# Kernel tuning notes

Hardware: AMD Instinct MI355X
Metric: run time of the kernel (lower is better)

## Reference

```python
import jax, jax.numpy as jnp
import numpy as np

IN, OUT, R, ALPHA = 4096, 4096, 32, 32
SCALE = ALPHA / R

def setup_inputs() -> dict:
    key = jax.random.key(0)
    k1, k2, k3, k4, k5 = jax.random.split(key, 5)
    x = jax.random.normal(k1, (4, 2048, IN), dtype=jnp.float32)
    weight = jax.random.normal(k2, (OUT, IN), dtype=jnp.float32) * 0.02
    bias = jax.random.normal(k3, (OUT,), dtype=jnp.float32) * 0.02
    A = jax.random.normal(k4, (OUT, R), dtype=jnp.float32) * 0.01
    # original init is zeros; use small randn so the LoRA path is nontrivial
    B = jax.random.normal(k5, (IN, R), dtype=jnp.float32) * 0.01
    return {"x": x, "weight": weight, "bias": bias, "A": A, "B": B}

def reference(x, weight, bias, A, B):
    # delta_w = A @ B.T * (alpha/r); y = x @ (W + delta_w).T + bias
    delta_w = (A @ B.T) * SCALE            # [out, in]
    w_eff = weight + delta_w
    return jnp.einsum('bsi,oi->bso', x, w_eff) + bias
```

## Files before the change

kernel.cpp:

```cpp
#include <hip/hip_runtime.h>

#define IN_DIM 4096
#define OUT_DIM 4096
#define M_DIM 8192
#define RANK 32
#define BK 64
#define NT (IN_DIM / BK)

typedef __bf16 bf16x8 __attribute__((ext_vector_type(8)));
typedef float f32x4 __attribute__((ext_vector_type(4)));

__device__ __forceinline__ unsigned short f2bf(float f) {
  unsigned u = __builtin_bit_cast(unsigned, f);
  u += 0x7FFF + ((u >> 16) & 1);
  return (unsigned short)(u >> 16);
}

__global__ __launch_bounds__(256) void prep_kernel(
    const float* __restrict__ X, unsigned short* __restrict__ Xb,
    const float* __restrict__ W, const float* __restrict__ A,
    const float* __restrict__ B, unsigned short* __restrict__ Wb) {
  const int tid = threadIdx.x;
  if (blockIdx.x >= 1024) {
    const int idx0 = (blockIdx.x - 1024) * 256 + tid;
    const int stride = 512 * 256;
    const int total4 = (M_DIM * IN_DIM) / 4;
    for (int i = idx0; i < total4; i += stride) {
      const float4 v = reinterpret_cast<const float4*>(X)[i];
      ushort4 o;
      o.x = f2bf(v.x); o.y = f2bf(v.y); o.z = f2bf(v.z); o.w = f2bf(v.w);
      reinterpret_cast<ushort4*>(Xb)[i] = o;
    }
    return;
  }
  __shared__ unsigned short sA[128][40];
  __shared__ unsigned short sB[128][40];
  const int lane = tid & 63;
  const int wid  = tid >> 6;
  const int wr   = wid >> 1, wc = wid & 1;
  const int li   = lane & 15, kg = lane >> 4;
  const int bRow = (blockIdx.x >> 5) * 128;
  const int bCol = (blockIdx.x & 31) * 128;

  for (int i = tid; i < 128 * 8; i += 256) {
    const int r = i >> 3, q = i & 7;
    const float4 va = reinterpret_cast<const float4*>(A + (size_t)(bRow + r) * RANK)[q];
    ushort4 oa;
    oa.x = f2bf(va.x); oa.y = f2bf(va.y); oa.z = f2bf(va.z); oa.w = f2bf(va.w);
    *reinterpret_cast<ushort4*>(&sA[r][q * 4]) = oa;
    const float4 vb = reinterpret_cast<const float4*>(B + (size_t)(bCol + r) * RANK)[q];
    ushort4 ob;
    ob.x = f2bf(vb.x); ob.y = f2bf(vb.y); ob.z = f2bf(vb.z); ob.w = f2bf(vb.w);
    *reinterpret_cast<ushort4*>(&sB[r][q * 4]) = ob;
  }
  __syncthreads();

  bf16x8 af[4], bq[4];
#pragma unroll
  for (int m = 0; m < 4; ++m)
    af[m] = *reinterpret_cast<const bf16x8*>(&sA[wr * 64 + m * 16 + li][kg * 8]);
#pragma unroll
  for (int n = 0; n < 4; ++n)
    bq[n] = *reinterpret_cast<const bf16x8*>(&sB[wc * 64 + n * 16 + li][kg * 8]);

  f32x4 acc[4][4];
#pragma unroll
  for (int m = 0; m < 4; ++m)
#pragma unroll
    for (int n = 0; n < 4; ++n) {
      acc[m][n] = f32x4{0.f, 0.f, 0.f, 0.f};
      acc[m][n] = __builtin_amdgcn_mfma_f32_16x16x32_bf16(af[m], bq[n], acc[m][n], 0, 0, 0);
    }

#pragma unroll
  for (int m = 0; m < 4; ++m) {
#pragma unroll
    for (int n = 0; n < 4; ++n) {
      const int col = bCol + wc * 64 + n * 16 + li;
#pragma unroll
      for (int j = 0; j < 4; ++j) {
        const int row = bRow + wr * 64 + m * 16 + kg * 4 + j;
        const size_t idx = (size_t)row * IN_DIM + col;
        Wb[idx] = f2bf(W[idx] + acc[m][n][j]);
      }
    }
  }
}

__global__ __launch_bounds__(512, 2) void gemm_kernel(
    const unsigned short* __restrict__ Xb, const unsigned short* __restrict__ Wb,
    const float* __restrict__ bias, float* __restrict__ Y) {
  __shared__ unsigned short lds[8][8192];
  const int tid  = threadIdx.x;
  const int lane = tid & 63;
  const int wid  = tid >> 6;
  const int wr   = wid >> 2;
  const int wc   = wid & 3;
  const int li   = lane & 15, kg = lane >> 4;

  const int bid = blockIdx.x;
  const int swz = (bid & 7) * 64 + (bid >> 3);
  const int bx  = swz & 15;
  const int by  = swz >> 4;
  const int bRow = by * 256, bCol = bx * 256;

  const int kcS = (tid & 7) ^ ((tid >> 3) & 7);
  const unsigned short* srcA[2][2];
  const unsigned short* srcB[2][2];
#pragma unroll
  for (int h = 0; h < 2; ++h)
#pragma unroll
    for (int l = 0; l < 2; ++l) {
      const int gA = l * 128 + h * 64 + (tid >> 3);
      const int gB = (l * 2 + (tid >> 8)) * 64 + h * 32 + ((tid >> 3) & 31);
      srcA[h][l] = Xb + (size_t)(bRow + gA) * IN_DIM + kcS * 8;
      srcB[h][l] = Wb + (size_t)(bCol + gB) * IN_DIM + kcS * 8;
    }
  char* const ldsRaw = (char*)&lds[0][0];

#define GLD(src, dstoff)                                                       \
  __builtin_amdgcn_global_load_lds(                                            \
      (const __attribute__((address_space(1))) unsigned int*)(src),            \
      (__attribute__((address_space(3))) unsigned int*)(ldsRaw + (dstoff)),    \
      16, 0, 0)
#define STAGE_A(s, h)                                                          \
  do {                                                                         \
    const int q_ = (((s) & 1) << 2) + (h);                                     \
    GLD(srcA[h][0] + (s) * BK, q_ * 16384 + tid * 16);                         \
    GLD(srcA[h][1] + (s) * BK, q_ * 16384 + 8192 + tid * 16);                  \
  } while (0)
#define STAGE_B(s, h)                                                          \
  do {                                                                         \
    const int q_ = (((s) & 1) << 2) + 2 + (h);                                 \
    GLD(srcB[h][0] + (s) * BK, q_ * 16384 + tid * 16);                         \
    GLD(srcB[h][1] + (s) * BK, q_ * 16384 + 8192 + tid * 16);                  \
  } while (0)
#define BAR() __builtin_amdgcn_s_barrier()

  const int rowAoff = (wr * 64 + li) * 64;
  const int rowBoff = (wc * 32 + li) * 64;
  int kx[2];
  kx[0] = ((0 * 4 + kg) ^ (li & 7)) * 8;
  kx[1] = ((1 * 4 + kg) ^ (li & 7)) * 8;

  bf16x8 af[4][2], bq[4][2];
  f32x4 acc[8][4];
#pragma unroll
  for (int m = 0; m < 8; ++m)
#pragma unroll
    for (int n = 0; n < 4; ++n) acc[m][n] = f32x4{0.f, 0.f, 0.f, 0.f};

#define RD_A(ms_)                                                              \
  do {                                                                         \
    const unsigned short* b_ = &lds[(dcur << 2) + (ms_)][0] + rowAoff;         \
    _Pragma("unroll") for (int mq = 0; mq < 4; ++mq)                           \
      _Pragma("unroll") for (int ks = 0; ks < 2; ++ks)                         \
        af[mq][ks] =                                                           \
            *reinterpret_cast<const bf16x8*>(b_ + mq * 1024 + kx[ks]);         \
  } while (0)
#define RD_B(ns_)                                                              \
  do {                                                                         \
    const unsigned short* b_ = &lds[(dcur << 2) + 2 + (ns_)][0] + rowBoff;     \
    _Pragma("unroll") for (int nq = 0; nq < 2; ++nq)                           \
      _Pragma("unroll") for (int ks = 0; ks < 2; ++ks)                         \
        bq[(ns_) * 2 + nq][ks] =                                               \
            *reinterpret_cast<const bf16x8*>(b_ + nq * 1024 + kx[ks]);         \
  } while (0)
#define MM(ms_, ns_)                                                           \
  do {                                                                         \
    __builtin_amdgcn_s_setprio(1);                                             \
    _Pragma("unroll") for (int mq = 0; mq < 4; ++mq)                           \
      _Pragma("unroll") for (int nq = 0; nq < 2; ++nq)                         \
        _Pragma("unroll") for (int ks = 0; ks < 2; ++ks)                       \
          acc[(ms_) * 4 + mq][(ns_) * 2 + nq] =                                \
              __builtin_amdgcn_mfma_f32_16x16x32_bf16(                         \
                  af[mq][ks], bq[(ns_) * 2 + nq][ks],                          \
                  acc[(ms_) * 4 + mq][(ns_) * 2 + nq], 0, 0, 0);               \
    __builtin_amdgcn_s_setprio(0);                                             \
  } while (0)

  STAGE_A(0, 0); STAGE_B(0, 0); STAGE_A(0, 1); STAGE_B(0, 1);
  STAGE_A(1, 0); STAGE_B(1, 0);
  asm volatile("s_waitcnt vmcnt(4)" ::: "memory");
  BAR();

  for (int t = 0; t < NT; ++t) {
    const int dcur = t & 1;
    const bool st1 = (t + 1 < NT), st2 = (t + 2 < NT);
    if (st1) { STAGE_B(t + 1, 1); STAGE_A(t + 1, 1); }
    RD_A(0); RD_B(0);
    BAR();
    MM(0, 0);
    RD_B(1);
    BAR();
    MM(0, 1);
    if (st2) STAGE_A(t + 2, 0);
    RD_A(1);
    BAR();
    MM(1, 0);
    if (st2) {
      STAGE_B(t + 2, 0);
      asm volatile("s_waitcnt vmcnt(4)" ::: "memory");
    } else {
      asm volatile("s_waitcnt vmcnt(0)" ::: "memory");
    }
    BAR();
    MM(1, 1);
  }
#undef GLD
#undef STAGE_A
#undef STAGE_B
#undef RD_A
#undef RD_B
#undef MM
#undef BAR

#pragma unroll
  for (int nf = 0; nf < 4; ++nf) {
    const int col = bCol + wc * 64 + nf * 16 + li;
    const float bv = bias[col];
#pragma unroll
    for (int mf = 0; mf < 8; ++mf) {
      const int row0 = bRow + wr * 128 + mf * 16 + kg * 4;
#pragma unroll
      for (int j = 0; j < 4; ++j)
        Y[(size_t)(row0 + j) * OUT_DIM + col] = acc[mf][nf][j] + bv;
    }
  }
}

extern "C" void kernel_launch(void* const* d_in, const int* in_sizes, int n_in,
                              void* d_out, int out_size, void* d_ws, size_t ws_size,
                              hipStream_t stream) {
  const float* x    = (const float*)d_in[0];
  const float* w    = (const float*)d_in[1];
  const float* bias = (const float*)d_in[2];
  const float* A    = (const float*)d_in[3];
  const float* B    = (const float*)d_in[4];
  float* y = (float*)d_out;

  const size_t xb_bytes = (size_t)M_DIM * IN_DIM * 2;
  const size_t wb_bytes = (size_t)OUT_DIM * IN_DIM * 2;
  if (ws_size < xb_bytes + wb_bytes) return;

  unsigned short* Xb = (unsigned short*)d_ws;
  unsigned short* Wb = (unsigned short*)((char*)d_ws + xb_bytes);

  prep_kernel<<<1536, 256, 0, stream>>>(x, Xb, w, A, B, Wb);
  gemm_kernel<<<(M_DIM / 256) * (OUT_DIM / 256), 512, 0, stream>>>(Xb, Wb, bias, y);
}
```

Baseline: 276.9 us.

## Split LDS fragment reads by k-substep and prefetch next tile into registers

Reorganizes the inner MFMA loop so A/B fragments are read per k-substep into two register sets and ping-ponged, with the first fragments of the next tile preloaded before the loop iteration ends. This aims to hide LDS read latency behind MFMA work across barrier phases. It also changes the vmcnt wait points and the ordering of global stage issues, which adds risk to the correctness of buffer reuse and raises register pressure.

```diff
diff --git a/kernel.cpp b/kernel.cpp
--- a/kernel.cpp
+++ b/kernel.cpp
@@ -143,39 +143,35 @@
   kx[0] = ((0 * 4 + kg) ^ (li & 7)) * 8;
   kx[1] = ((1 * 4 + kg) ^ (li & 7)) * 8;
 
-  bf16x8 af[4][2], bq[4][2];
+  bf16x8 af0[4], af1[4], bq0[4], bq1[4];
   f32x4 acc[8][4];
 #pragma unroll
   for (int m = 0; m < 8; ++m)
 #pragma unroll
     for (int n = 0; n < 4; ++n) acc[m][n] = f32x4{0.f, 0.f, 0.f, 0.f};
 
-#define RD_A(ms_)                                                              \
-  do {                                                                         \
-    const unsigned short* b_ = &lds[(dcur << 2) + (ms_)][0] + rowAoff;         \
+#define RD_AF(dst, dsel, h, ks)                                                \
+  do {                                                                         \
+    const unsigned short* a_ = &lds[((dsel) << 2) + (h)][0] + rowAoff;         \
     _Pragma("unroll") for (int mq = 0; mq < 4; ++mq)                           \
-      _Pragma("unroll") for (int ks = 0; ks < 2; ++ks)                         \
-        af[mq][ks] =                                                           \
-            *reinterpret_cast<const bf16x8*>(b_ + mq * 1024 + kx[ks]);         \
-  } while (0)
-#define RD_B(ns_)                                                              \
-  do {                                                                         \
-    const unsigned short* b_ = &lds[(dcur << 2) + 2 + (ns_)][0] + rowBoff;     \
-    _Pragma("unroll") for (int nq = 0; nq < 2; ++nq)                           \
-      _Pragma("unroll") for (int ks = 0; ks < 2; ++ks)                         \
-        bq[(ns_) * 2 + nq][ks] =                                               \
-            *reinterpret_cast<const bf16x8*>(b_ + nq * 1024 + kx[ks]);         \
-  } while (0)
-#define MM(ms_, ns_)                                                           \
+      dst[mq] = *reinterpret_cast<const bf16x8*>(a_ + mq * 1024 + kx[ks]);     \
+  } while (0)
+#define RD_BQ(dst, dsel, ks)                                                   \
+  do {                                                                         \
+    const unsigned short* b0_ = &lds[((dsel) << 2) + 2][0] + rowBoff;          \
+    const unsigned short* b1_ = &lds[((dsel) << 2) + 3][0] + rowBoff;          \
+    dst[0] = *reinterpret_cast<const bf16x8*>(b0_ + kx[ks]);                   \
+    dst[1] = *reinterpret_cast<const bf16x8*>(b0_ + 1024 + kx[ks]);            \
+    dst[2] = *reinterpret_cast<const bf16x8*>(b1_ + kx[ks]);                   \
+    dst[3] = *reinterpret_cast<const bf16x8*>(b1_ + 1024 + kx[ks]);            \
+  } while (0)
+#define MM(base, afv, bqv)                                                     \
   do {                                                                         \
     __builtin_amdgcn_s_setprio(1);                                             \
     _Pragma("unroll") for (int mq = 0; mq < 4; ++mq)                           \
-      _Pragma("unroll") for (int nq = 0; nq < 2; ++nq)                         \
-        _Pragma("unroll") for (int ks = 0; ks < 2; ++ks)                       \
-          acc[(ms_) * 4 + mq][(ns_) * 2 + nq] =                                \
-              __builtin_amdgcn_mfma_f32_16x16x32_bf16(                         \
-                  af[mq][ks], bq[(ns_) * 2 + nq][ks],                          \
-                  acc[(ms_) * 4 + mq][(ns_) * 2 + nq], 0, 0, 0);               \
+      _Pragma("unroll") for (int nq = 0; nq < 4; ++nq)                         \
+        acc[(base) + mq][nq] = __builtin_amdgcn_mfma_f32_16x16x32_bf16(        \
+            afv[mq], bqv[nq], acc[(base) + mq][nq], 0, 0, 0);                  \
     __builtin_amdgcn_s_setprio(0);                                             \
   } while (0)
 
@@ -183,37 +179,39 @@
   STAGE_A(1, 0); STAGE_B(1, 0);
   asm volatile("s_waitcnt vmcnt(4)" ::: "memory");
   BAR();
+  RD_AF(af0, 0, 0, 0);
+  RD_BQ(bq0, 0, 0);
 
   for (int t = 0; t < NT; ++t) {
     const int dcur = t & 1;
+    const int dn   = dcur ^ 1;
     const bool st1 = (t + 1 < NT), st2 = (t + 2 < NT);
     if (st1) { STAGE_B(t + 1, 1); STAGE_A(t + 1, 1); }
-    RD_A(0); RD_B(0);
-    BAR();
-    MM(0, 0);
-    RD_B(1);
-    BAR();
-    MM(0, 1);
+    RD_AF(af1, dcur, 0, 1);
+    RD_BQ(bq1, dcur, 1);
+    BAR();
+    MM(0, af0, bq0);
+    RD_AF(af0, dcur, 1, 0);
+    BAR();
+    MM(0, af1, bq1);
     if (st2) STAGE_A(t + 2, 0);
-    RD_A(1);
-    BAR();
-    MM(1, 0);
-    if (st2) {
-      STAGE_B(t + 2, 0);
-      asm volatile("s_waitcnt vmcnt(4)" ::: "memory");
-    } else {
-      asm volatile("s_waitcnt vmcnt(0)" ::: "memory");
-    }
-    BAR();
-    MM(1, 1);
+    RD_AF(af1, dcur, 1, 1);
+    if (st2) asm volatile("s_waitcnt vmcnt(2)" ::: "memory");
+    else     asm volatile("s_waitcnt vmcnt(0)" ::: "memory");
+    BAR();
+    MM(4, af0, bq0);
+    if (st2) STAGE_B(t + 2, 0);
+    if (st1) { RD_AF(af0, dn, 0, 0); RD_BQ(bq0, dn, 0); }
+    BAR();
+    MM(4, af1, bq1);
   }
 #undef GLD
 #undef STAGE_A
 #undef STAGE_B
-#undef RD_A
-#undef RD_B
+#undef BAR
+#undef RD_AF
+#undef RD_BQ
 #undef MM
-#undef BAR
 
 #pragma unroll
   for (int nf = 0; nf < 4; ++nf) {
```

New measurement: 280.3 us. Within noise of the previous version (+1.2%).

## Fuse X fp32-to-bf16 conversion into GEMM A-tile loading via registers

Applied to the files above, without the earlier changes.

Removes the separate pass that converted X to bf16 in a workspace. The GEMM now loads fp32 X into registers, converts to bf16 and writes to LDS, while W still uses direct global-to-LDS loads. This avoids writing and rereading a bf16 copy of X. In exchange, every tile reload fetches twice the bytes, and the kernel gains extra VALU conversion work and register pressure in the main loop.

```diff
diff --git a/kernel.cpp b/kernel.cpp
--- a/kernel.cpp
+++ b/kernel.cpp
@@ -9,6 +9,7 @@
 
 typedef __bf16 bf16x8 __attribute__((ext_vector_type(8)));
 typedef float f32x4 __attribute__((ext_vector_type(4)));
+typedef unsigned short u16x8 __attribute__((ext_vector_type(8)));
 
 __device__ __forceinline__ unsigned short f2bf(float f) {
   unsigned u = __builtin_bit_cast(unsigned, f);
@@ -17,22 +18,9 @@
 }
 
 __global__ __launch_bounds__(256) void prep_kernel(
-    const float* __restrict__ X, unsigned short* __restrict__ Xb,
     const float* __restrict__ W, const float* __restrict__ A,
     const float* __restrict__ B, unsigned short* __restrict__ Wb) {
   const int tid = threadIdx.x;
-  if (blockIdx.x >= 1024) {
-    const int idx0 = (blockIdx.x - 1024) * 256 + tid;
-    const int stride = 512 * 256;
-    const int total4 = (M_DIM * IN_DIM) / 4;
-    for (int i = idx0; i < total4; i += stride) {
-      const float4 v = reinterpret_cast<const float4*>(X)[i];
-      ushort4 o;
-      o.x = f2bf(v.x); o.y = f2bf(v.y); o.z = f2bf(v.z); o.w = f2bf(v.w);
-      reinterpret_cast<ushort4*>(Xb)[i] = o;
-    }
-    return;
-  }
   __shared__ unsigned short sA[128][40];
   __shared__ unsigned short sB[128][40];
   const int lane = tid & 63;
@@ -88,7 +76,7 @@
 }
 
 __global__ __launch_bounds__(512, 2) void gemm_kernel(
-    const unsigned short* __restrict__ Xb, const unsigned short* __restrict__ Wb,
+    const float* __restrict__ Xf, const unsigned short* __restrict__ Wb,
     const float* __restrict__ bias, float* __restrict__ Y) {
   __shared__ unsigned short lds[8][8192];
   const int tid  = threadIdx.x;
@@ -105,7 +93,7 @@
   const int bRow = by * 256, bCol = bx * 256;
 
   const int kcS = (tid & 7) ^ ((tid >> 3) & 7);
-  const unsigned short* srcA[2][2];
+  const float* srcAf[2][2];
   const unsigned short* srcB[2][2];
 #pragma unroll
   for (int h = 0; h < 2; ++h)
@@ -113,8 +101,8 @@
     for (int l = 0; l < 2; ++l) {
       const int gA = l * 128 + h * 64 + (tid >> 3);
       const int gB = (l * 2 + (tid >> 8)) * 64 + h * 32 + ((tid >> 3) & 31);
-      srcA[h][l] = Xb + (size_t)(bRow + gA) * IN_DIM + kcS * 8;
-      srcB[h][l] = Wb + (size_t)(bCol + gB) * IN_DIM + kcS * 8;
+      srcAf[h][l] = Xf + (size_t)(bRow + gA) * IN_DIM + kcS * 8;
+      srcB[h][l]  = Wb + (size_t)(bCol + gB) * IN_DIM + kcS * 8;
     }
   char* const ldsRaw = (char*)&lds[0][0];
 
@@ -123,19 +111,36 @@
       (const __attribute__((address_space(1))) unsigned int*)(src),            \
       (__attribute__((address_space(3))) unsigned int*)(ldsRaw + (dstoff)),    \
       16, 0, 0)
-#define STAGE_A(s, h)                                                          \
-  do {                                                                         \
-    const int q_ = (((s) & 1) << 2) + (h);                                     \
-    GLD(srcA[h][0] + (s) * BK, q_ * 16384 + tid * 16);                         \
-    GLD(srcA[h][1] + (s) * BK, q_ * 16384 + 8192 + tid * 16);                  \
-  } while (0)
 #define STAGE_B(s, h)                                                          \
   do {                                                                         \
     const int q_ = (((s) & 1) << 2) + 2 + (h);                                 \
     GLD(srcB[h][0] + (s) * BK, q_ * 16384 + tid * 16);                         \
     GLD(srcB[h][1] + (s) * BK, q_ * 16384 + 8192 + tid * 16);                  \
   } while (0)
+#define A_LOAD(vv, s, h)                                                       \
+  do {                                                                         \
+    vv[0] = *reinterpret_cast<const float4*>(srcAf[h][0] + (s) * BK);          \
+    vv[1] = *reinterpret_cast<const float4*>(srcAf[h][0] + (s) * BK + 4);      \
+    vv[2] = *reinterpret_cast<const float4*>(srcAf[h][1] + (s) * BK);          \
+    vv[3] = *reinterpret_cast<const float4*>(srcAf[h][1] + (s) * BK + 4);      \
+  } while (0)
+#define A_WRITE(vv, s, h)                                                      \
+  do {                                                                         \
+    const int q_ = (((s) & 1) << 2) + (h);                                     \
+    u16x8 o0_, o1_;                                                            \
+    o0_[0] = f2bf(vv[0].x); o0_[1] = f2bf(vv[0].y);                            \
+    o0_[2] = f2bf(vv[0].z); o0_[3] = f2bf(vv[0].w);                            \
+    o0_[4] = f2bf(vv[1].x); o0_[5] = f2bf(vv[1].y);                            \
+    o0_[6] = f2bf(vv[1].z); o0_[7] = f2bf(vv[1].w);                            \
+    o1_[0] = f2bf(vv[2].x); o1_[1] = f2bf(vv[2].y);                            \
+    o1_[2] = f2bf(vv[2].z); o1_[3] = f2bf(vv[2].w);                            \
+    o1_[4] = f2bf(vv[3].x); o1_[5] = f2bf(vv[3].y);                            \
+    o1_[6] = f2bf(vv[3].z); o1_[7] = f2bf(vv[3].w);                            \
+    *reinterpret_cast<u16x8*>(ldsRaw + q_ * 16384 + tid * 16) = o0_;           \
+    *reinterpret_cast<u16x8*>(ldsRaw + q_ * 16384 + 8192 + tid * 16) = o1_;    \
+  } while (0)
 #define BAR() __builtin_amdgcn_s_barrier()
+#define SB()  __builtin_amdgcn_sched_barrier(0)
 
   const int rowAoff = (wr * 64 + li) * 64;
   const int rowBoff = (wc * 32 + li) * 64;
@@ -144,6 +149,7 @@
   kx[1] = ((1 * 4 + kg) ^ (li & 7)) * 8;
 
   bf16x8 af[4][2], bq[4][2];
+  float4 a0v[4], a1v[4];
   f32x4 acc[8][4];
 #pragma unroll
   for (int m = 0; m < 8; ++m)
@@ -179,41 +185,54 @@
     __builtin_amdgcn_s_setprio(0);                                             \
   } while (0)
 
-  STAGE_A(0, 0); STAGE_B(0, 0); STAGE_A(0, 1); STAGE_B(0, 1);
-  STAGE_A(1, 0); STAGE_B(1, 0);
-  asm volatile("s_waitcnt vmcnt(4)" ::: "memory");
+  A_LOAD(a0v, 0, 0);
+  A_LOAD(a1v, 0, 1);
+  STAGE_B(0, 0); STAGE_B(0, 1);
+  SB();
+  A_WRITE(a0v, 0, 0);
+  A_WRITE(a1v, 0, 1);
+  SB();
+  A_LOAD(a0v, 1, 0);
+  STAGE_B(1, 0);
+  asm volatile("s_waitcnt vmcnt(6)" ::: "memory");
   BAR();
 
   for (int t = 0; t < NT; ++t) {
     const int dcur = t & 1;
     const bool st1 = (t + 1 < NT), st2 = (t + 2 < NT);
-    if (st1) { STAGE_B(t + 1, 1); STAGE_A(t + 1, 1); }
+    if (st1) { STAGE_B(t + 1, 1); A_LOAD(a1v, t + 1, 1); }
     RD_A(0); RD_B(0);
     BAR();
     MM(0, 0);
     RD_B(1);
     BAR();
     MM(0, 1);
-    if (st2) STAGE_A(t + 2, 0);
+    SB();
+    if (st1) A_WRITE(a0v, t + 1, 0);
+    if (st2) A_LOAD(a0v, t + 2, 0);
     RD_A(1);
     BAR();
     MM(1, 0);
+    SB();
+    if (st2) STAGE_B(t + 2, 0);
+    if (st1) A_WRITE(a1v, t + 1, 1);
     if (st2) {
-      STAGE_B(t + 2, 0);
-      asm volatile("s_waitcnt vmcnt(4)" ::: "memory");
-    } else {
+      asm volatile("s_waitcnt vmcnt(6)" ::: "memory");
+    } else if (st1) {
       asm volatile("s_waitcnt vmcnt(0)" ::: "memory");
     }
     BAR();
     MM(1, 1);
   }
 #undef GLD
-#undef STAGE_A
 #undef STAGE_B
+#undef A_LOAD
+#undef A_WRITE
 #undef RD_A
 #undef RD_B
 #undef MM
 #undef BAR
+#undef SB
 
 #pragma unroll
   for (int nf = 0; nf < 4; ++nf) {
@@ -239,13 +258,11 @@
   const float* B    = (const float*)d_in[4];
   float* y = (float*)d_out;
 
-  const size_t xb_bytes = (size_t)M_DIM * IN_DIM * 2;
   const size_t wb_bytes = (size_t)OUT_DIM * IN_DIM * 2;
-  if (ws_size < xb_bytes + wb_bytes) return;
-
-  unsigned short* Xb = (unsigned short*)d_ws;
-  unsigned short* Wb = (unsigned short*)((char*)d_ws + xb_bytes);
-
-  prep_kernel<<<1536, 256, 0, stream>>>(x, Xb, w, A, B, Wb);
-  gemm_kernel<<<(M_DIM / 256) * (OUT_DIM / 256), 512, 0, stream>>>(Xb, Wb, bias, y);
-}
+  if (ws_size < wb_bytes) return;
+
+  unsigned short* Wb = (unsigned short*)d_ws;
+
+  prep_kernel<<<1024, 256, 0, stream>>>(w, A, B, Wb);
+  gemm_kernel<<<(M_DIM / 256) * (OUT_DIM / 256), 512, 0, stream>>>(x, Wb, bias, y);
+}
```

New measurement: 320.9 us. +15.9%, slower.
